# Kernel tuning notes

Hardware: AMD Instinct MI355X
Metric: run time of the kernel (lower is better)

The kernel has to match this reference:

```python
import jax, jax.numpy as jnp
import numpy as np


def setup_inputs() -> dict:
    key = jax.random.key(0)
    kx, kz = jax.random.split(key)
    B, H, W = 4, 512, 2048
    x = jax.random.normal(kx, (B, 1, H, W), dtype=jnp.float32)
    z = jax.random.uniform(kz, (B, 1, H, W), dtype=jnp.float32)
    return {"x": x, "z": z, "w_ceil": 16}


def reference(x, z, w_ceil):
    # The two structured sparse conv2d's reduce exactly to:
    #   z_exp[b,i,h,j] = z[b,0,h,j-i]            (eye_filter: right-shift, zero pad)
    #   out[b,i,h,j]   = (x*z_exp)[b,i,h,j+i]    (delay kernel + slice: left-shift, zero pad)
    # => out[b,i,h,j] = x[b,0,h,j+i] * z[b,0,h,j], zero where j+i >= W.
    B, _, H, W = x.shape
    shifts = jnp.arange(w_ceil)                       # [w]
    idx = jnp.arange(W)[None, :] + shifts[:, None]    # [w, W], value j+i
    valid = (idx < W)[None, :, None, :]               # [1, w, 1, W]
    idx = jnp.minimum(idx, W - 1)                     # clamp, masked below
    xg = jnp.take(x[:, 0], idx, axis=-1)              # [B, H, w, W]
    xg = jnp.transpose(xg, (0, 2, 1, 3))              # [B, w, H, W]
    out = jnp.where(valid, xg * z, jnp.zeros((), x.dtype))  # z broadcasts over channel dim
    return out
```

## Files before the change

kernel.cpp:

```cpp
#include <hip/hip_runtime.h>


#define B_ 4
#define H_ 512
#define W_ 2048
#define WC_ 16

__global__ __launch_bounds__(256) void
space2features_kernel(const float* __restrict__ x,
                      const float* __restrict__ z,
                      float* __restrict__ out) {
    const int tid = blockIdx.x * blockDim.x + threadIdx.x;
    const int JV = W_ / 4;
    const int jv = tid & (JV - 1);
    const int bh = tid >> 9;
    if (bh >= B_ * H_) return;
    const int j = jv * 4;

    const float* xrow = x + (size_t)bh * W_;
    const float* zrow = z + (size_t)bh * W_;

    const float4 z4 = *(const float4*)(zrow + j);

    float xr[20];
    const long long gbase = (long long)bh * W_ + j;
    const long long total = (long long)B_ * H_ * W_;
    if (gbase + 20 <= total) {
#pragma unroll
        for (int k = 0; k < 5; ++k) {
            float4 t = *(const float4*)(xrow + j + 4 * k);
            xr[4 * k + 0] = t.x;
            xr[4 * k + 1] = t.y;
            xr[4 * k + 2] = t.z;
            xr[4 * k + 3] = t.w;
        }
    } else {
#pragma unroll
        for (int k = 0; k < 20; ++k) {
            xr[k] = (gbase + k < total) ? xrow[j + k] : 0.0f;
        }
    }

    const int b = bh >> 9;
    const int h = bh & (H_ - 1);
    float* obase = out + (((size_t)b * WC_) * H_ + h) * (size_t)W_ + j;

#pragma unroll
    for (int i = 0; i < WC_; ++i) {
        float4 o;
        o.x = (j + 0 + i < W_) ? xr[i + 0] * z4.x : 0.0f;
        o.y = (j + 1 + i < W_) ? xr[i + 1] * z4.y : 0.0f;
        o.z = (j + 2 + i < W_) ? xr[i + 2] * z4.z : 0.0f;
        o.w = (j + 3 + i < W_) ? xr[i + 3] * z4.w : 0.0f;
        *(float4*)(obase + (size_t)i * (H_ * W_)) = o;
    }
}

extern "C" void kernel_launch(void* const* d_in, const int* in_sizes, int n_in,
                              void* d_out, int out_size, void* d_ws, size_t ws_size,
                              hipStream_t stream) {
    const float* x = (const float*)d_in[0];
    const float* z = (const float*)d_in[1];
    float* out = (float*)d_out;

    const int total_threads = B_ * H_ * (W_ / 4);
    const int block = 256;
    const int grid = (total_threads + block - 1) / block;
    space2features_kernel<<<grid, block, 0, stream>>>(x, z, out);
}
```

Baseline: 294.6 us.

## Map one block per output row instead of per input row segment

Reorganizes the grid so each block writes one contiguous output row (b, i, h) of 2048 floats, with each thread handling two float4 chunks. Each thread now reloads x with scalar, possibly unaligned, shifted reads per output channel rather than reusing a 20-element register window across all 16 channels. The aim is fully contiguous per-block stores and more blocks in flight. The cost is roughly 16x more x and z load traffic, which should mostly hit in cache, and scalar gather-style loads.

```diff
diff --git a/kernel.cpp b/kernel.cpp
--- a/kernel.cpp
+++ b/kernel.cpp
@@ -10,49 +10,36 @@
 space2features_kernel(const float* __restrict__ x,
                       const float* __restrict__ z,
                       float* __restrict__ out) {
-    const int tid = blockIdx.x * blockDim.x + threadIdx.x;
-    const int JV = W_ / 4;
-    const int jv = tid & (JV - 1);
-    const int bh = tid >> 9;
-    if (bh >= B_ * H_) return;
-    const int j = jv * 4;
+    const int blk = blockIdx.x;
+    const int h = blk & (H_ - 1);
+    const int i = (blk >> 9) & (WC_ - 1);
+    const int b = blk >> 13;
 
-    const float* xrow = x + (size_t)bh * W_;
-    const float* zrow = z + (size_t)bh * W_;
+    const size_t inrow = ((size_t)(b * H_ + h)) * W_;
+    const float* __restrict__ xr = x + inrow;
+    const float* __restrict__ zr = z + inrow;
+    float* __restrict__ orow = out + (size_t)blk * W_;
 
-    const float4 z4 = *(const float4*)(zrow + j);
-
-    float xr[20];
-    const long long gbase = (long long)bh * W_ + j;
-    const long long total = (long long)B_ * H_ * W_;
-    if (gbase + 20 <= total) {
-#pragma unroll
-        for (int k = 0; k < 5; ++k) {
-            float4 t = *(const float4*)(xrow + j + 4 * k);
-            xr[4 * k + 0] = t.x;
-            xr[4 * k + 1] = t.y;
-            xr[4 * k + 2] = t.z;
-            xr[4 * k + 3] = t.w;
-        }
-    } else {
-#pragma unroll
-        for (int k = 0; k < 20; ++k) {
-            xr[k] = (gbase + k < total) ? xrow[j + k] : 0.0f;
-        }
-    }
-
-    const int b = bh >> 9;
-    const int h = bh & (H_ - 1);
-    float* obase = out + (((size_t)b * WC_) * H_ + h) * (size_t)W_ + j;
+    const int t = threadIdx.x;
 
 #pragma unroll
-    for (int i = 0; i < WC_; ++i) {
+    for (int half = 0; half < 2; ++half) {
+        const int j = half * 1024 + t * 4;
+        const float4 z4 = *(const float4*)(zr + j);
+
         float4 o;
-        o.x = (j + 0 + i < W_) ? xr[i + 0] * z4.x : 0.0f;
-        o.y = (j + 1 + i < W_) ? xr[i + 1] * z4.y : 0.0f;
-        o.z = (j + 2 + i < W_) ? xr[i + 2] * z4.z : 0.0f;
-        o.w = (j + 3 + i < W_) ? xr[i + 3] * z4.w : 0.0f;
-        *(float4*)(obase + (size_t)i * (H_ * W_)) = o;
+        {
+            const int ji = j + i;
+            const float x0 = xr[min(ji + 0, W_ - 1)];
+            const float x1 = xr[min(ji + 1, W_ - 1)];
+            const float x2 = xr[min(ji + 2, W_ - 1)];
+            const float x3 = xr[min(ji + 3, W_ - 1)];
+            o.x = (ji + 0 < W_) ? x0 * z4.x : 0.0f;
+            o.y = (ji + 1 < W_) ? x1 * z4.y : 0.0f;
+            o.z = (ji + 2 < W_) ? x2 * z4.z : 0.0f;
+            o.w = (ji + 3 < W_) ? x3 * z4.w : 0.0f;
+        }
+        *(float4*)(orow + j) = o;
     }
 }
 
@@ -63,8 +50,6 @@
     const float* z = (const float*)d_in[1];
     float* out = (float*)d_out;
 
-    const int total_threads = B_ * H_ * (W_ / 4);
-    const int block = 256;
-    const int grid = (total_threads + block - 1) / block;
-    space2features_kernel<<<grid, block, 0, stream>>>(x, z, out);
+    const int grid = B_ * WC_ * H_;
+    space2features_kernel<<<grid, 256, 0, stream>>>(x, z, out);
 }
```

After: 312.3 us. 1.06x slower.
